# Kernel optimization log

Hardware: AMD Instinct MI355X
Metric: run time of the kernel (lower is better)

The kernel has to match this reference:

```python
import jax, jax.numpy as jnp
import numpy as np

HEADS = 4
KNN_K = 20
BN_EPS = 1e-5


def conv1x1(w, b, x):
    # 1x1 Conv1d: w [out, in], x [B, in, N] -> [B, out, N]
    return jnp.einsum('oc,bcn->bon', w, x) + b[None, :, None]


def setup_inputs() -> dict:
    key = jax.random.key(0)
    B, C, N = 2, 128, 2048
    ks = jax.random.split(key, 16)
    W = lambda k, o, i: jax.random.normal(k, (o, i), jnp.float32) * 0.05
    V = lambda k, o: jax.random.normal(k, (o,), jnp.float32) * 0.05
    return {
        'desc1': jax.random.normal(ks[0], (B, C, N, 1), jnp.float32),
        'wq': W(ks[1], C, C), 'bq': V(ks[2], C),
        'wk': W(ks[3], C, C), 'bk': V(ks[4], C),
        'wv': W(ks[5], C, C), 'bv': V(ks[6], C),
        'wm': W(ks[7], C, C), 'bm': V(ks[8], C),
        'w1': W(ks[9], 2 * C, 2 * C), 'b1': V(ks[10], 2 * C),
        'gamma': jnp.ones((2 * C,), jnp.float32),
        'beta': jnp.zeros((2 * C,), jnp.float32),
        'w2': W(ks[11], C, 2 * C), 'b2': V(ks[12], C),
    }


def reference(desc1, wq, bq, wk, bk, wv, bv, wm, bm, w1, b1, gamma, beta, w2, b2):
    x = desc1[..., 0]                      # [B, C, N]
    B, C, N = x.shape
    D = C // HEADS

    q = conv1x1(wq, bq, x).reshape(B, HEADS, D, N)
    k = conv1x1(wk, bk, x).reshape(B, HEADS, D, N)
    v = conv1x1(wv, bv, x).reshape(B, HEADS, D, N)

    # kNN on raw descriptors: pd = -||xi||^2 + 2 xi.xj - ||xj||^2 (larger = closer)
    xx = jnp.sum(x * x, axis=1)            # [B, N]
    pd = 2.0 * jnp.einsum('bcn,bcm->bnm', x, x) - xx[:, :, None] - xx[:, None, :]
    idx = jax.lax.top_k(pd, KNN_K)[1]      # [B, N, K]

    # scatter ones at kNN indices, then keep only mutual neighbors
    bI = jnp.arange(B)[:, None, None]
    nI = jnp.arange(N)[None, :, None]
    mask = jnp.zeros((B, N, N), x.dtype).at[bI, nI, idx].set(1.0)
    mask = mask * mask.transpose(0, 2, 1)  # [B, N, N]

    score = jnp.einsum('bhdn,bhdm->bhnm', q, k) / (D ** 0.5)
    m = mask[:, None]                      # broadcast over heads
    score = score * m + (-1e9) * (1.0 - m)
    score = jax.nn.softmax(score, axis=-1)

    av = jnp.einsum('bhnm,bhdm->bhdn', score, v).reshape(B, C, N)
    av = conv1x1(wm, bm, av)

    h = conv1x1(w1, b1, jnp.concatenate([x, av], axis=1))  # [B, 2C, N]
    mu = jnp.mean(h, axis=(0, 2), keepdims=True)
    var = jnp.var(h, axis=(0, 2), keepdims=True)           # biased, matches torch BN
    h = (h - mu) / jnp.sqrt(var + BN_EPS) * gamma[None, :, None] + beta[None, :, None]
    h = jax.nn.relu(h)

    out = x + conv1x1(w2, b2, h)
    return out[..., None]                  # [B, C, N, 1]
```

## Files before the change

### kernel.cpp

```cpp
#include <hip/hip_runtime.h>
#include <math.h>

#define NPT 2048
#define KNN 20

typedef const float* fp;
typedef __attribute__((ext_vector_type(4))) float f32x4;
typedef __attribute__((ext_vector_type(8))) short s16x8;

__device__ __forceinline__ ushort f2bf_rne(float v) {
    unsigned u = __float_as_uint(v);
    unsigned r = u + 0x7FFFu + ((u >> 16) & 1u);
    return (ushort)(r >> 16);
}
__device__ __forceinline__ float bfbits2f(ushort h) {
    return __uint_as_float(((unsigned)h) << 16);
}
__device__ __forceinline__ s16x8 ldfrag(const ushort* p) {
    union { uint4 u; s16x8 s; } cv;
    cv.u = *reinterpret_cast<const uint4*>(p);
    return cv.s;
}
__device__ __forceinline__ void f8_hilo(const float* row, s16x8* hi, s16x8* lo) {
    float4 f0 = *reinterpret_cast<const float4*>(row);
    float4 f1 = *reinterpret_cast<const float4*>(row + 4);
    float f[8] = {f0.x, f0.y, f0.z, f0.w, f1.x, f1.y, f1.z, f1.w};
    union { ushort u[8]; s16x8 s; } H, L;
    #pragma unroll
    for (int j = 0; j < 8; j++) {
        ushort h = f2bf_rne(f[j]);
        H.u[j] = h;
        L.u[j] = f2bf_rne(f[j] - bfbits2f(h));
    }
    *hi = H.s; *lo = L.s;
}

__global__ __launch_bounds__(256) void prep_all(
    fp xbf, fp wq, fp wk, fp wv, fp wm, fp w1, fp w2, fp bm, fp b1,
    float* xx, ushort* xhiF, ushort* xloF,
    ushort* wqFhi, ushort* wqFlo, ushort* wkFhi, ushort* wkFlo,
    ushort* wvFhi, ushort* wvFlo,
    ushort* wcFhi, ushort* wcFlo, ushort* w2Fhi, ushort* w2Flo,
    float* b1p, float* stats) {
    int t = threadIdx.x;
    if (blockIdx.x < 256) {
        __shared__ float xs[16][129];
        __shared__ float xpart[16][17];
        int p0 = blockIdx.x * 16;
        int b = p0 >> 11, n0 = p0 & 2047;
        fp xb = xbf + (size_t)b * 128 * NPT;
        {
            int c = t >> 1, half = t & 1;
            float4 f0 = *reinterpret_cast<const float4*>(xb + (size_t)c * NPT + n0 + half * 8);
            float4 f1 = *reinterpret_cast<const float4*>(xb + (size_t)c * NPT + n0 + half * 8 + 4);
            xs[half * 8 + 0][c] = f0.x; xs[half * 8 + 1][c] = f0.y;
            xs[half * 8 + 2][c] = f0.z; xs[half * 8 + 3][c] = f0.w;
            xs[half * 8 + 4][c] = f1.x; xs[half * 8 + 5][c] = f1.y;
            xs[half * 8 + 6][c] = f1.z; xs[half * 8 + 7][c] = f1.w;
        }
        __syncthreads();
        int p = t & 15, g = t >> 4, c0 = g * 8;
        float f[8];
        #pragma unroll
        for (int j = 0; j < 8; j++) f[j] = xs[p][c0 + j];
        float ps = 0.f;
        #pragma unroll
        for (int j = 0; j < 8; j++) ps += f[j] * f[j];
        xpart[p][g] = ps;
        union { ushort u[8]; uint4 q; } H, L;
        #pragma unroll
        for (int j = 0; j < 8; j++) {
            ushort hi = f2bf_rne(f[j]);
            H.u[j] = hi;
            L.u[j] = f2bf_rne(f[j] - bfbits2f(hi));
        }
        size_t off = ((size_t)blockIdx.x * 4 + (c0 >> 5)) * 512
                   + (size_t)(((((c0 >> 3) & 3) * 16) + p) * 8);
        *reinterpret_cast<uint4*>(xhiF + off) = H.q;
        *reinterpret_cast<uint4*>(xloF + off) = L.q;
        __syncthreads();
        if (t < 16) {
            float s = 0.f;
            #pragma unroll
            for (int gg = 0; gg < 16; gg++) s += xpart[t][gg];
            xx[p0 + t] = s;
        }
        return;
    }
    int wid = (blockIdx.x - 256) * 256 + t;
    if (wid < 49152) {
        int which = wid >> 14, e = wid & 16383;
        int lane = (e >> 3) & 63, j = e & 7, kk = (e >> 9) & 3, nt = e >> 11;
        int n = nt * 16 + (lane & 15);
        int k = kk * 32 + (lane >> 4) * 8 + j;
        fp src = which == 0 ? wq : which == 1 ? wk : wv;
        float v = src[n * 128 + k];
        ushort hi = f2bf_rne(v);
        (which == 0 ? wqFhi : which == 1 ? wkFhi : wvFhi)[e] = hi;
        (which == 0 ? wqFlo : which == 1 ? wkFlo : wvFlo)[e] = f2bf_rne(v - bfbits2f(hi));
    } else if (wid < 114688) {
        int e = wid - 49152;
        int j = e & 7, lane = (e >> 3) & 63, kk = (e >> 9) & 7, nt = e >> 12;
        int n = nt * 16 + (lane & 15);
        int k = kk * 32 + (lane >> 4) * 8 + j;
        float v;
        if (k < 128) {
            v = w1[n * 256 + k];
        } else {
            int c = k - 128;
            float s = 0.f;
            for (int i = 0; i < 128; i += 4) {
                float4 wr = *reinterpret_cast<const float4*>(w1 + n * 256 + 128 + i);
                s += wr.x * wm[(i + 0) * 128 + c];
                s += wr.y * wm[(i + 1) * 128 + c];
                s += wr.z * wm[(i + 2) * 128 + c];
                s += wr.w * wm[(i + 3) * 128 + c];
            }
            v = s;
        }
        ushort hi = f2bf_rne(v);
        wcFhi[e] = hi;
        wcFlo[e] = f2bf_rne(v - bfbits2f(hi));
    } else if (wid < 147456) {
        int e = wid - 114688;
        int j = e & 7, lane = (e >> 3) & 63, kk = (e >> 9) & 7, nt = e >> 12;
        int n = nt * 16 + (lane & 15);
        int k = kk * 32 + (lane >> 4) * 8 + j;
        float v = w2[n * 256 + k];
        ushort hi = f2bf_rne(v);
        w2Fhi[e] = hi;
        w2Flo[e] = f2bf_rne(v - bfbits2f(hi));
    } else if (wid < 147712) {
        int o = wid - 147456;
        float s = b1[o];
        for (int i = 0; i < 128; i++)
            s += w1[o * 256 + 128 + i] * bm[i];
        b1p[o] = s;
    } else {
        stats[wid - 147712] = 0.0f;
    }
}

#define MERGE(off) { float ov = __shfl_xor(bv, off); int oi = __shfl_xor(bi, off); \
                     if (ov > bv || (ov == bv && oi < bi)) { bv = ov; bi = oi; } }

#define KEYTILE(C, DST) { \
    int ctl = half * 64 + w * 4 + C; \
    int ct = slab * 128 + ctl; \
    f32x4 a = (f32x4){0.f, 0.f, 0.f, 0.f}; \
    _Pragma("unroll 2") \
    for (int kk = 0; kk < 4; kk++) { \
        s16x8 ah = ldfrag(Ahi[kk] + lane * 8); \
        s16x8 al = ldfrag(Alo[kk] + lane * 8); \
        s16x8 bh = ldfrag(xhiF + ((size_t)(ct * 4 + kk)) * 512 + lane * 8); \
        s16x8 bl = ldfrag(xloF + ((size_t)(ct * 4 + kk)) * 512 + lane * 8); \
        a = __builtin_amdgcn_mfma_f32_16x16x32_bf16(ah, bh, a, 0, 0, 0); \
        a = __builtin_amdgcn_mfma_f32_16x16x32_bf16(al, bh, a, 0, 0, 0); \
        a = __builtin_amdgcn_mfma_f32_16x16x32_bf16(ah, bl, a, 0, 0, 0); \
    } \
    float xxc = xx[slab * 2048 + ctl * 16 + cl]; \
    a[0] = 2.0f * a[0] - xxc; a[1] = 2.0f * a[1] - xxc; \
    a[2] = 2.0f * a[2] - xxc; a[3] = 2.0f * a[3] - xxc; \
    DST = a; \
}

__global__ __launch_bounds__(1024, 8) void gemm_key_topk(
    const ushort* xhiF, const ushort* xloF, const float* xx,
    const ushort* wqFhi, const ushort* wqFlo,
    const ushort* wkFhi, const ushort* wkFlo,
    const ushort* wvFhi, const ushort* wvFlo,
    fp bq, fp bk, fp bv_, float* qT, float* kT, float* vT,
    float* pvv, int* pii, int* cntb, float* scratch) {
    __shared__ ushort Ahi[4][512];
    __shared__ ushort Alo[4][512];
    __shared__ float chm[16][32];
    __shared__ float sv[16][256];
    __shared__ int   si[16][256];
    __shared__ float Trow[16];
    __shared__ int   rowcnt[16];
    __shared__ int   ovfAll;
    int tt = threadIdx.x, w = tt >> 6, lane = tt & 63;
    int rt = blockIdx.x >> 1, half = blockIdx.x & 1;
    int slab = rt >> 7, rtl = rt & 127;
    int cl = lane & 15, quad = lane >> 4;

    if (tt < 16) rowcnt[tt] = 0;

    if (tt < 512) {
        int which = tt >> 8, kk = (tt >> 6) & 3, ln = tt & 63;
        const ushort* src = (which ? xloF : xhiF)
                          + ((size_t)(rt * 4 + kk)) * 512 + ln * 8;
        uint4 v = *reinterpret_cast<const uint4*>(src);
        *reinterpret_cast<uint4*>((which ? Alo[kk] : Ahi[kk]) + ln * 8) = v;
    }
    __syncthreads();

    if (w < 12) {
        int pair = half * 12 + w;
        int mat = pair >> 3, nt = pair & 7;
        const ushort* whi = mat == 0 ? wqFhi : mat == 1 ? wkFhi : wvFhi;
        const ushort* wlo = mat == 0 ? wqFlo : mat == 1 ? wkFlo : wvFlo;
        f32x4 acc = (f32x4){0.f, 0.f, 0.f, 0.f};
        #pragma unroll 2
        for (int kk = 0; kk < 4; kk++) {
            s16x8 ah = ldfrag(Ahi[kk] + lane * 8);
            s16x8 al = ldfrag(Alo[kk] + lane * 8);
            s16x8 bhi = ldfrag(whi + ((size_t)(nt * 4 + kk)) * 512 + lane * 8);
            s16x8 blo = ldfrag(wlo + ((size_t)(nt * 4 + kk)) * 512 + lane * 8);
            acc = __builtin_amdgcn_mfma_f32_16x16x32_bf16(ah, bhi, acc, 0, 0, 0);
            acc = __builtin_amdgcn_mfma_f32_16x16x32_bf16(al, bhi, acc, 0, 0, 0);
            acc = __builtin_amdgcn_mfma_f32_16x16x32_bf16(ah, blo, acc, 0, 0, 0);
        }
        int p0 = rt * 16;
        fp bias    = mat == 0 ? bq : mat == 1 ? bk : bv_;
        float* out = mat == 0 ? qT : mat == 1 ? kT : vT;
        int o = nt * 16 + cl;
        float bvv = bias[o];
        #pragma unroll
        for (int r = 0; r < 4; r++)
            out[(size_t)(p0 + quad * 4 + r) * 128 + o] = acc[r] + bvv;
    }
    __builtin_amdgcn_sched_barrier(0);

    f32x4 key0, key1, key2, key3;
    KEYTILE(0, key0)
    __builtin_amdgcn_sched_barrier(0);
    KEYTILE(1, key1)
    __builtin_amdgcn_sched_barrier(0);
    KEYTILE(2, key2)
    __builtin_amdgcn_sched_barrier(0);
    KEYTILE(3, key3)
    __builtin_amdgcn_sched_barrier(0);

    {
        float m[4];
        #pragma unroll
        for (int r = 0; r < 4; r++) {
            float mm = fmaxf(fmaxf(key0[r], key1[r]), fmaxf(key2[r], key3[r]));
            mm = fmaxf(mm, __shfl_xor(mm, 1));
            mm = fmaxf(mm, __shfl_xor(mm, 2));
            mm = fmaxf(mm, __shfl_xor(mm, 4));
            m[r] = mm;
        }
        if ((cl & 7) == 0) {
            #pragma unroll
            for (int r = 0; r < 4; r++)
                chm[quad * 4 + r][w * 2 + (cl >> 3)] = m[r];
        }
    }
    __syncthreads();

    {
        float bs = (lane < 32) ? chm[w][lane] : -3.4e38f;
        #pragma unroll
        for (int k = 2; k <= 64; k <<= 1) {
            #pragma unroll
            for (int j = k >> 1; j > 0; j >>= 1) {
                float o = __shfl_xor(bs, j);
                bool dirDesc = (lane & k) != 0;
                bool upper   = (lane & j) != 0;
                bs = (upper != dirDesc) ? fmaxf(bs, o) : fminf(bs, o);
            }
        }
        float T = __shfl(bs, 44);
        if (lane == 0) Trow[w] = T;
    }
    __syncthreads();

    #pragma unroll
    for (int r = 0; r < 4; r++) {
        int row = quad * 4 + r;
        float T = Trow[row];
        float vals[4] = {key0[r], key1[r], key2[r], key3[r]};
        #pragma unroll
        for (int c = 0; c < 4; c++) {
            float v = vals[c];
            if (v >= T) {
                int pos = atomicAdd(&rowcnt[row], 1);
                if (pos < 256) {
                    sv[row][pos] = v;
                    si[row][pos] = (half * 64 + w * 4 + c) * 16 + cl;
                }
            }
        }
    }
    __syncthreads();
    if (tt == 0) {
        int o = 0;
        for (int i = 0; i < 16; i++) o |= (rowcnt[i] > 256) ? 1 : 0;
        ovfAll = o;
    }
    __syncthreads();
    int ovf = ovfAll;

    int S = rowcnt[w];
    int rowg = slab * 2048 + rtl * 16 + w;
    size_t sbase = ((size_t)rowg * 2 + half) * 256;
    if (S <= 256) {
        if (lane == 0) cntb[rowg * 2 + half] = S;
        for (int g = lane; g < S; g += 64) {
            pvv[sbase + g] = sv[w][g];
            pii[sbase + g] = si[w][g];
        }
    }

    if (ovf) {
        #pragma unroll
        for (int r = 0; r < 4; r++) {
            float vals[4] = {key0[r], key1[r], key2[r], key3[r]};
            #pragma unroll
            for (int c = 0; c < 4; c++)
                scratch[((size_t)rt * 16 + quad * 4 + r) * 2048
                        + (half * 64 + w * 4 + c) * 16 + cl] = vals[c];
        }
        __syncthreads();
        if (rowcnt[w] > 256) {
            const float* rowp = scratch + ((size_t)rt * 16 + w) * 2048 + half * 1024;
            float rv[16];
            #pragma unroll
            for (int j = 0; j < 16; j++) rv[j] = rowp[j * 64 + lane];
            unsigned removed = 0u;
            for (int iter = 0; iter < KNN; iter++) {
                float bv = -3.4e38f; int bi = 0;
                #pragma unroll
                for (int sl = 0; sl < 16; sl++) {
                    bool live = ((removed >> sl) & 1u) == 0u;
                    if (live && rv[sl] > bv) {
                        bv = rv[sl]; bi = half * 1024 + sl * 64 + lane;
                    }
                }
                MERGE(32) MERGE(16) MERGE(8) MERGE(4) MERGE(2) MERGE(1)
                if (lane == 0) { pvv[sbase + iter] = bv; pii[sbase + iter] = bi; }
                if ((bi & 63) == lane) removed |= 1u << ((bi - half * 1024) >> 6);
            }
            if (lane == 0) cntb[rowg * 2 + half] = -1;
        }
    }
}

__global__ __launch_bounds__(256) void sort_topk(
    const float* pvv, const int* pii, const int* cntb, int* idxbuf) {
    int w = threadIdx.x >> 6, lane = threadIdx.x & 63;
    int row = blockIdx.x * 4 + w;
    int c0 = cntb[row * 2 + 0], c1 = cntb[row * 2 + 1];
    if (c0 < 0) c0 = KNN;
    if (c1 < 0) c1 = KNN;
    int Stot = c0 + c1;
    const float* v0 = pvv + ((size_t)row * 2 + 0) * 256;
    const float* v1 = pvv + ((size_t)row * 2 + 1) * 256;
    const int*   i0 = pii + ((size_t)row * 2 + 0) * 256;
    const int*   i1 = pii + ((size_t)row * 2 + 1) * 256;
    if (Stot <= 64) {
        float v; int idx;
        if (lane < c0)        { v = v0[lane];      idx = i0[lane]; }
        else if (lane < Stot) { v = v1[lane - c0]; idx = i1[lane - c0]; }
        else                  { v = -3.4e38f;      idx = 0x7FFFFFFF; }
        #pragma unroll
        for (int k = 2; k <= 64; k <<= 1) {
            #pragma unroll
            for (int j = k >> 1; j > 0; j >>= 1) {
                float ov = __shfl_xor(v, j); int oi = __shfl_xor(idx, j);
                bool dirDesc = (lane & k) != 0;
                bool upper   = (lane & j) != 0;
                bool takeMax = (upper != dirDesc);
                bool amax = (v > ov) || (v == ov && idx < oi);
                if (takeMax != amax) { v = ov; idx = oi; }
            }
        }
        if (lane >= 44) idxbuf[(size_t)row * KNN + (63 - lane)] = idx;
    } else {
        float vl[8]; int il[8];
        #pragma unroll
        for (int s = 0; s < 8; s++) {
            int g = lane + s * 64;
            float v = -3.4e38f; int idx = 0x7FFFFFFF;
            if (g < c0)        { v = v0[g];      idx = i0[g]; }
            else if (g < Stot) { v = v1[g - c0]; idx = i1[g - c0]; }
            vl[s] = v; il[s] = idx;
        }
        unsigned removed = 0u;
        for (int iter = 0; iter < KNN; iter++) {
            float bv = -3.4e38f; int bi = 0x7FFFFFFF;
            #pragma unroll
            for (int s = 0; s < 8; s++) {
                bool live = ((removed >> s) & 1u) == 0u;
                if (live && (vl[s] > bv || (vl[s] == bv && il[s] < bi))) {
                    bv = vl[s]; bi = il[s];
                }
            }
            MERGE(32) MERGE(16) MERGE(8) MERGE(4) MERGE(2) MERGE(1)
            if (lane == 0) idxbuf[(size_t)row * KNN + iter] = bi;
            #pragma unroll
            for (int s = 0; s < 8; s++)
                if (il[s] == bi) removed |= 1u << s;
        }
    }
}

__global__ __launch_bounds__(256) void k3_attn(
    fp qT, fp kT, fp vT, const int* idxbuf, float* avT) {
    __shared__ float sbuf[2][KNN * 4];
    __shared__ int   mlist[2][KNN];
    __shared__ int   cnt_s[2];
    int tt = threadIdx.x;
    int half = tt >> 7, t = tt & 127;
    int p = blockIdx.x * 2 + half;
    int b = p >> 11, n = p & 2047;
    int bbase = b * NPT;
    int h = t >> 5;

    if ((tt >> 6) == half * 2) {
        int lane = tt & 63;
        bool fl = false; int m = 0;
        if (lane < KNN) {
            m = idxbuf[(size_t)p * KNN + lane] & 2047;
            const int4* mrow = reinterpret_cast<const int4*>(idxbuf + (size_t)(bbase + m) * KNN);
            int4 r0 = mrow[0], r1 = mrow[1], r2 = mrow[2], r3 = mrow[3], r4 = mrow[4];
            fl = (r0.x == n) || (r0.y == n) || (r0.z == n) || (r0.w == n)
              || (r1.x == n) || (r1.y == n) || (r1.z == n) || (r1.w == n)
              || (r2.x == n) || (r2.y == n) || (r2.z == n) || (r2.w == n)
              || (r3.x == n) || (r3.y == n) || (r3.z == n) || (r3.w == n)
              || (r4.x == n) || (r4.y == n) || (r4.z == n) || (r4.w == n);
        }
        unsigned long long mask = __ballot(fl);
        int pos = __popcll(mask & ((1ull << lane) - 1ull));
        if (fl) mlist[half][pos] = m;
        if (lane == 0) cnt_s[half] = (int)__popcll(mask);
    }
    __syncthreads();

    int cnt = cnt_s[half];
    float qv = qT[(size_t)p * 128 + t];
    for (int jj = 0; jj < cnt; jj++) {
        int m = mlist[half][jj];
        float prod = qv * kT[(size_t)(bbase + m) * 128 + t];
        prod += __shfl_xor(prod, 16);
        prod += __shfl_xor(prod, 8);
        prod += __shfl_xor(prod, 4);
        prod += __shfl_xor(prod, 2);
        prod += __shfl_xor(prod, 1);
        if ((t & 31) == 0) sbuf[half][jj * 4 + h] = prod * 0.17677669529663687f;
    }
    __syncthreads();

    float mx = -3.4e38f;
    for (int j = 0; j < cnt; j++) mx = fmaxf(mx, sbuf[half][j * 4 + h]);
    float den = 0.f;
    for (int j = 0; j < cnt; j++) den += expf(sbuf[half][j * 4 + h] - mx);
    float inv = (cnt > 0) ? (1.0f / den) : 0.0f;
    float acc = 0.f;
    for (int j = 0; j < cnt; j++) {
        float pw = expf(sbuf[half][j * 4 + h] - mx) * inv;
        acc += pw * vT[(size_t)(bbase + mlist[half][j]) * 128 + t];
    }
    avT[(size_t)p * 128 + t] = acc;
}

__global__ __launch_bounds__(1024) void k4b_h(
    const ushort* xhiF, const ushort* xloF, const float* avT,
    const ushort* wcFhi, const ushort* wcFlo,
    const float* b1p, float* hbuf, float* stats) {
    __shared__ ushort AH[8][512];
    __shared__ ushort AL[8][512];
    int tt = threadIdx.x, w = tt >> 6, lane = tt & 63;
    int rt = blockIdx.x;
    int p0 = rt * 16;

    if (w < 8) {
        int which = w & 1, kk = w >> 1;
        const ushort* src = (which ? xloF : xhiF)
                          + ((size_t)(rt * 4 + kk)) * 512 + lane * 8;
        uint4 v = *reinterpret_cast<const uint4*>(src);
        *reinterpret_cast<uint4*>((which ? AL[kk] : AH[kk]) + lane * 8) = v;
    } else if (w < 12) {
        int kk = 4 + (w - 8);
        const float* arow = avT + (size_t)(p0 + (lane & 15)) * 128
                          + (kk - 4) * 32 + (lane >> 4) * 8;
        s16x8 hi, lo;
        f8_hilo(arow, &hi, &lo);
        union { s16x8 s; uint4 u; } cvh, cvl;
        cvh.s = hi; cvl.s = lo;
        *reinterpret_cast<uint4*>(AH[kk] + lane * 8) = cvh.u;
        *reinterpret_cast<uint4*>(AL[kk] + lane * 8) = cvl.u;
    }
    __syncthreads();

    int nt = w;
    f32x4 acc = (f32x4){0.f, 0.f, 0.f, 0.f};
    for (int kk = 0; kk < 8; kk++) {
        s16x8 ahi = ldfrag(AH[kk] + lane * 8);
        s16x8 alo = ldfrag(AL[kk] + lane * 8);
        s16x8 bhi = ldfrag(wcFhi + ((size_t)(nt * 8 + kk)) * 512 + lane * 8);
        s16x8 blo = ldfrag(wcFlo + ((size_t)(nt * 8 + kk)) * 512 + lane * 8);
        acc = __builtin_amdgcn_mfma_f32_16x16x32_bf16(ahi, bhi, acc, 0, 0, 0);
        acc = __builtin_amdgcn_mfma_f32_16x16x32_bf16(alo, bhi, acc, 0, 0, 0);
        acc = __builtin_amdgcn_mfma_f32_16x16x32_bf16(ahi, blo, acc, 0, 0, 0);
    }

    int cl = lane & 15, quad = lane >> 4;
    int o = nt * 16 + cl;
    float bb = b1p[o];
    float s = 0.f, s2 = 0.f;
    #pragma unroll
    for (int r = 0; r < 4; r++) {
        float v = acc[r] + bb;
        hbuf[(size_t)(p0 + quad * 4 + r) * 256 + o] = v;
        s += v; s2 += v * v;
    }
    s  += __shfl_xor(s, 16);  s  += __shfl_xor(s, 32);
    s2 += __shfl_xor(s2, 16); s2 += __shfl_xor(s2, 32);
    if (quad == 0) {
        atomicAdd(&stats[o], s);
        atomicAdd(&stats[256 + o], s2);
    }
}

__global__ __launch_bounds__(512) void k5b_out(
    const float* hbuf, const float* stats, fp gamma, fp beta,
    const ushort* w2Fhi, const ushort* w2Flo,
    fp b2, fp xbf, float* out) {
    __shared__ ushort HH[8][512];
    __shared__ ushort HL[8][512];
    int tt = threadIdx.x, w = tt >> 6, lane = tt & 63;
    int rt = blockIdx.x;
    int p0 = rt * 16;

    {
        int kk = w;
        int c0 = kk * 32 + (lane >> 4) * 8;
        const float* hrow = hbuf + (size_t)(p0 + (lane & 15)) * 256 + c0;
        float4 f0 = *reinterpret_cast<const float4*>(hrow);
        float4 f1 = *reinterpret_cast<const float4*>(hrow + 4);
        float4 s0 = *reinterpret_cast<const float4*>(stats + c0);
        float4 s1 = *reinterpret_cast<const float4*>(stats + c0 + 4);
        float4 q0 = *reinterpret_cast<const float4*>(stats + 256 + c0);
        float4 q1 = *reinterpret_cast<const float4*>(stats + 256 + c0 + 4);
        float4 g0 = *reinterpret_cast<const float4*>(gamma + c0);
        float4 g1 = *reinterpret_cast<const float4*>(gamma + c0 + 4);
        float4 e0 = *reinterpret_cast<const float4*>(beta + c0);
        float4 e1 = *reinterpret_cast<const float4*>(beta + c0 + 4);
        float f[8] = {f0.x, f0.y, f0.z, f0.w, f1.x, f1.y, f1.z, f1.w};
        float sm[8] = {s0.x, s0.y, s0.z, s0.w, s1.x, s1.y, s1.z, s1.w};
        float sq[8] = {q0.x, q0.y, q0.z, q0.w, q1.x, q1.y, q1.z, q1.w};
        float gm[8] = {g0.x, g0.y, g0.z, g0.w, g1.x, g1.y, g1.z, g1.w};
        float bt[8] = {e0.x, e0.y, e0.z, e0.w, e1.x, e1.y, e1.z, e1.w};
        union { ushort u[8]; uint4 q; } H, L;
        #pragma unroll
        for (int j = 0; j < 8; j++) {
            float mu  = sm[j] * (1.0f / 4096.0f);
            float var = fmaxf(sq[j] * (1.0f / 4096.0f) - mu * mu, 0.0f);
            float a    = gm[j] / sqrtf(var + 1e-5f);
            float cadd = bt[j] - mu * a;
            float v = fmaxf(f[j] * a + cadd, 0.0f);
            ushort hi = f2bf_rne(v);
            H.u[j] = hi;
            L.u[j] = f2bf_rne(v - bfbits2f(hi));
        }
        *reinterpret_cast<uint4*>(HH[kk] + lane * 8) = H.q;
        *reinterpret_cast<uint4*>(HL[kk] + lane * 8) = L.q;
    }
    __syncthreads();

    int nt = w;
    f32x4 acc = (f32x4){0.f, 0.f, 0.f, 0.f};
    for (int kk = 0; kk < 8; kk++) {
        s16x8 ahi = ldfrag(HH[kk] + lane * 8);
        s16x8 alo = ldfrag(HL[kk] + lane * 8);
        s16x8 bhi = ldfrag(w2Fhi + ((size_t)(nt * 8 + kk)) * 512 + lane * 8);
        s16x8 blo = ldfrag(w2Flo + ((size_t)(nt * 8 + kk)) * 512 + lane * 8);
        acc = __builtin_amdgcn_mfma_f32_16x16x32_bf16(ahi, bhi, acc, 0, 0, 0);
        acc = __builtin_amdgcn_mfma_f32_16x16x32_bf16(alo, bhi, acc, 0, 0, 0);
        acc = __builtin_amdgcn_mfma_f32_16x16x32_bf16(ahi, blo, acc, 0, 0, 0);
    }
    int cl = lane & 15, quad = lane >> 4;
    int b = p0 >> 11, n0 = p0 & 2047;
    int o = nt * 16 + cl;
    float bb = b2[o];
    size_t base = (size_t)b * 128 * NPT + (size_t)o * NPT + n0 + quad * 4;
    float4 xv = *reinterpret_cast<const float4*>(xbf + base);
    float4 ov;
    ov.x = acc[0] + bb + xv.x;
    ov.y = acc[1] + bb + xv.y;
    ov.z = acc[2] + bb + xv.z;
    ov.w = acc[3] + bb + xv.w;
    *reinterpret_cast<float4*>(out + base) = ov;
}

#define WS_FULL 61788160u

extern "C" void kernel_launch(void* const* d_in, const int* in_sizes, int n_in,
                              void* d_out, int out_size, void* d_ws, size_t ws_size,
                              hipStream_t stream) {
    fp desc1 = (fp)d_in[0];
    fp wq = (fp)d_in[1];  fp bq = (fp)d_in[2];
    fp wk = (fp)d_in[3];  fp bk = (fp)d_in[4];
    fp wv = (fp)d_in[5];  fp bv = (fp)d_in[6];
    fp wm = (fp)d_in[7];  fp bm = (fp)d_in[8];
    fp w1 = (fp)d_in[9];  fp b1 = (fp)d_in[10];
    fp gamma = (fp)d_in[11]; fp beta = (fp)d_in[12];
    fp w2 = (fp)d_in[13]; fp b2 = (fp)d_in[14];

    if (ws_size < (size_t)WS_FULL) return;

    char* ws = (char*)d_ws;
    float*  qT    = (float*) (ws + 0);
    float*  kT    = (float*) (ws + 2097152);
    float*  vT    = (float*) (ws + 4194304);
    float*  avT   = (float*) (ws + 6291456);
    float*  xx    = (float*) (ws + 8388608);
    int*    idxb  = (int*)   (ws + 8404992);
    float*  stats = (float*) (ws + 8732672);
    float*  b1p   = (float*) (ws + 8734720);
    ushort* wqFhi = (ushort*)(ws + 8736768);
    ushort* wqFlo = (ushort*)(ws + 8769536);
    ushort* wkFhi = (ushort*)(ws + 8802304);
    ushort* wkFlo = (ushort*)(ws + 8835072);
    ushort* wvFhi = (ushort*)(ws + 8867840);
    ushort* wvFlo = (ushort*)(ws + 8900608);
    ushort* wcFhi = (ushort*)(ws + 8933376);
    ushort* wcFlo = (ushort*)(ws + 9064448);
    ushort* w2Fhi = (ushort*)(ws + 9195520);
    ushort* w2Flo = (ushort*)(ws + 9261056);
    ushort* xhiF  = (ushort*)(ws + 9326592);
    ushort* xloF  = (ushort*)(ws + 10375168);
    int*    cntb  = (int*)   (ws + 11423744);
    float*  pvv   = (float*) (ws + 11456512);
    int*    pii   = (int*)   (ws + 19845120);
    float*  scratch = (float*)(ws + 28233728);
    float*  hbuf  = (float*) (ws + 0);

    prep_all<<<835, 256, 0, stream>>>(desc1, wq, wk, wv, wm, w1, w2, bm, b1,
                                      xx, xhiF, xloF,
                                      wqFhi, wqFlo, wkFhi, wkFlo, wvFhi, wvFlo,
                                      wcFhi, wcFlo, w2Fhi, w2Flo, b1p, stats);
    gemm_key_topk<<<512, 1024, 0, stream>>>(xhiF, xloF, xx,
                                            wqFhi, wqFlo, wkFhi, wkFlo,
                                            wvFhi, wvFlo,
                                            bq, bk, bv, qT, kT, vT,
                                            pvv, pii, cntb, scratch);
    sort_topk<<<1024, 256, 0, stream>>>(pvv, pii, cntb, idxb);
    k3_attn<<<2048, 256, 0, stream>>>(qT, kT, vT, idxb, avT);
    k4b_h<<<256, 1024, 0, stream>>>(xhiF, xloF, avT, wcFhi, wcFlo,
                                    b1p, hbuf, stats);
    k5b_out<<<256, 512, 0, stream>>>(hbuf, stats, gamma, beta, w2Fhi, w2Flo,
                                     b2, desc1, (float*)d_out);
}
```

Measured before the change: 186.1 us.

## Merge half-row key blocks into one block covering full 2048-column row

Each gemm_key_topk block now computes all 2048 key columns for its 16 rows instead of splitting them across two blocks. Each wave handles two column tiles per MFMA pass, sharing the A fragments. The threshold now comes from 64 chunk maxima instead of 32, and each row writes a single candidate list, so sort_topk no longer merges two halves. The grid halves to 256 blocks with launch bounds lowered to 4, which trades parallelism and occupancy for fewer redundant A loads and a cheaper merge stage, plus possibly more candidates per row.

```diff
diff --git a/kernel.cpp b/kernel.cpp
--- a/kernel.cpp
+++ b/kernel.cpp
@@ -144,27 +144,36 @@
 #define MERGE(off) { float ov = __shfl_xor(bv, off); int oi = __shfl_xor(bi, off); \
                      if (ov > bv || (ov == bv && oi < bi)) { bv = ov; bi = oi; } }
 
-#define KEYTILE(C, DST) { \
-    int ctl = half * 64 + w * 4 + C; \
-    int ct = slab * 128 + ctl; \
-    f32x4 a = (f32x4){0.f, 0.f, 0.f, 0.f}; \
+#define KEYPAIR(C0, D0, D1) { \
+    int ct0 = slab * 128 + w * 8 + C0; \
+    int ct1 = ct0 + 1; \
+    f32x4 a0 = (f32x4){0.f, 0.f, 0.f, 0.f}; \
+    f32x4 a1 = (f32x4){0.f, 0.f, 0.f, 0.f}; \
     _Pragma("unroll 2") \
     for (int kk = 0; kk < 4; kk++) { \
         s16x8 ah = ldfrag(Ahi[kk] + lane * 8); \
         s16x8 al = ldfrag(Alo[kk] + lane * 8); \
-        s16x8 bh = ldfrag(xhiF + ((size_t)(ct * 4 + kk)) * 512 + lane * 8); \
-        s16x8 bl = ldfrag(xloF + ((size_t)(ct * 4 + kk)) * 512 + lane * 8); \
-        a = __builtin_amdgcn_mfma_f32_16x16x32_bf16(ah, bh, a, 0, 0, 0); \
-        a = __builtin_amdgcn_mfma_f32_16x16x32_bf16(al, bh, a, 0, 0, 0); \
-        a = __builtin_amdgcn_mfma_f32_16x16x32_bf16(ah, bl, a, 0, 0, 0); \
+        s16x8 b0h = ldfrag(xhiF + ((size_t)(ct0 * 4 + kk)) * 512 + lane * 8); \
+        s16x8 b0l = ldfrag(xloF + ((size_t)(ct0 * 4 + kk)) * 512 + lane * 8); \
+        s16x8 b1h = ldfrag(xhiF + ((size_t)(ct1 * 4 + kk)) * 512 + lane * 8); \
+        s16x8 b1l = ldfrag(xloF + ((size_t)(ct1 * 4 + kk)) * 512 + lane * 8); \
+        a0 = __builtin_amdgcn_mfma_f32_16x16x32_bf16(ah, b0h, a0, 0, 0, 0); \
+        a1 = __builtin_amdgcn_mfma_f32_16x16x32_bf16(ah, b1h, a1, 0, 0, 0); \
+        a0 = __builtin_amdgcn_mfma_f32_16x16x32_bf16(al, b0h, a0, 0, 0, 0); \
+        a1 = __builtin_amdgcn_mfma_f32_16x16x32_bf16(al, b1h, a1, 0, 0, 0); \
+        a0 = __builtin_amdgcn_mfma_f32_16x16x32_bf16(ah, b0l, a0, 0, 0, 0); \
+        a1 = __builtin_amdgcn_mfma_f32_16x16x32_bf16(ah, b1l, a1, 0, 0, 0); \
     } \
-    float xxc = xx[slab * 2048 + ctl * 16 + cl]; \
-    a[0] = 2.0f * a[0] - xxc; a[1] = 2.0f * a[1] - xxc; \
-    a[2] = 2.0f * a[2] - xxc; a[3] = 2.0f * a[3] - xxc; \
-    DST = a; \
-}
-
-__global__ __launch_bounds__(1024, 8) void gemm_key_topk(
+    float xx0 = xx[slab * 2048 + (w * 8 + C0) * 16 + cl]; \
+    float xx1 = xx[slab * 2048 + (w * 8 + C0 + 1) * 16 + cl]; \
+    a0[0] = 2.0f * a0[0] - xx0; a0[1] = 2.0f * a0[1] - xx0; \
+    a0[2] = 2.0f * a0[2] - xx0; a0[3] = 2.0f * a0[3] - xx0; \
+    a1[0] = 2.0f * a1[0] - xx1; a1[1] = 2.0f * a1[1] - xx1; \
+    a1[2] = 2.0f * a1[2] - xx1; a1[3] = 2.0f * a1[3] - xx1; \
+    D0 = a0; D1 = a1; \
+}
+
+__global__ __launch_bounds__(1024, 4) void gemm_key_topk(
     const ushort* xhiF, const ushort* xloF, const float* xx,
     const ushort* wqFhi, const ushort* wqFlo,
     const ushort* wkFhi, const ushort* wkFlo,
@@ -173,14 +182,14 @@
     float* pvv, int* pii, int* cntb, float* scratch) {
     __shared__ ushort Ahi[4][512];
     __shared__ ushort Alo[4][512];
-    __shared__ float chm[16][32];
+    __shared__ float chm[16][64];
     __shared__ float sv[16][256];
     __shared__ int   si[16][256];
     __shared__ float Trow[16];
     __shared__ int   rowcnt[16];
     __shared__ int   ovfAll;
     int tt = threadIdx.x, w = tt >> 6, lane = tt & 63;
-    int rt = blockIdx.x >> 1, half = blockIdx.x & 1;
+    int rt = blockIdx.x;
     int slab = rt >> 7, rtl = rt & 127;
     int cl = lane & 15, quad = lane >> 4;
 
@@ -196,62 +205,82 @@
     __syncthreads();
 
     if (w < 12) {
-        int pair = half * 12 + w;
-        int mat = pair >> 3, nt = pair & 7;
-        const ushort* whi = mat == 0 ? wqFhi : mat == 1 ? wkFhi : wvFhi;
-        const ushort* wlo = mat == 0 ? wqFlo : mat == 1 ? wkFlo : wvFlo;
-        f32x4 acc = (f32x4){0.f, 0.f, 0.f, 0.f};
+        f32x4 acc0 = (f32x4){0.f, 0.f, 0.f, 0.f};
+        f32x4 acc1 = (f32x4){0.f, 0.f, 0.f, 0.f};
+        int pair0 = w * 2, pair1 = w * 2 + 1;
+        int mat0 = pair0 >> 3, nt0 = pair0 & 7;
+        int mat1 = pair1 >> 3, nt1 = pair1 & 7;
+        const ushort* w0hi = mat0 == 0 ? wqFhi : mat0 == 1 ? wkFhi : wvFhi;
+        const ushort* w0lo = mat0 == 0 ? wqFlo : mat0 == 1 ? wkFlo : wvFlo;
+        const ushort* w1hi = mat1 == 0 ? wqFhi : mat1 == 1 ? wkFhi : wvFhi;
+        const ushort* w1lo = mat1 == 0 ? wqFlo : mat1 == 1 ? wkFlo : wvFlo;
         #pragma unroll 2
         for (int kk = 0; kk < 4; kk++) {
             s16x8 ah = ldfrag(Ahi[kk] + lane * 8);
             s16x8 al = ldfrag(Alo[kk] + lane * 8);
-            s16x8 bhi = ldfrag(whi + ((size_t)(nt * 4 + kk)) * 512 + lane * 8);
-            s16x8 blo = ldfrag(wlo + ((size_t)(nt * 4 + kk)) * 512 + lane * 8);
-            acc = __builtin_amdgcn_mfma_f32_16x16x32_bf16(ah, bhi, acc, 0, 0, 0);
-            acc = __builtin_amdgcn_mfma_f32_16x16x32_bf16(al, bhi, acc, 0, 0, 0);
-            acc = __builtin_amdgcn_mfma_f32_16x16x32_bf16(ah, blo, acc, 0, 0, 0);
+            s16x8 b0h = ldfrag(w0hi + ((size_t)(nt0 * 4 + kk)) * 512 + lane * 8);
+            s16x8 b0l = ldfrag(w0lo + ((size_t)(nt0 * 4 + kk)) * 512 + lane * 8);
+            s16x8 b1h = ldfrag(w1hi + ((size_t)(nt1 * 4 + kk)) * 512 + lane * 8);
+            s16x8 b1l = ldfrag(w1lo + ((size_t)(nt1 * 4 + kk)) * 512 + lane * 8);
+            acc0 = __builtin_amdgcn_mfma_f32_16x16x32_bf16(ah, b0h, acc0, 0, 0, 0);
+            acc1 = __builtin_amdgcn_mfma_f32_16x16x32_bf16(ah, b1h, acc1, 0, 0, 0);
+            acc0 = __builtin_amdgcn_mfma_f32_16x16x32_bf16(al, b0h, acc0, 0, 0, 0);
+            acc1 = __builtin_amdgcn_mfma_f32_16x16x32_bf16(al, b1h, acc1, 0, 0, 0);
+            acc0 = __builtin_amdgcn_mfma_f32_16x16x32_bf16(ah, b0l, acc0, 0, 0, 0);
+            acc1 = __builtin_amdgcn_mfma_f32_16x16x32_bf16(ah, b1l, acc1, 0, 0, 0);
         }
         int p0 = rt * 16;
-        fp bias    = mat == 0 ? bq : mat == 1 ? bk : bv_;
-        float* out = mat == 0 ? qT : mat == 1 ? kT : vT;
-        int o = nt * 16 + cl;
-        float bvv = bias[o];
-        #pragma unroll
-        for (int r = 0; r < 4; r++)
-            out[(size_t)(p0 + quad * 4 + r) * 128 + o] = acc[r] + bvv;
+        {
+            fp bias    = mat0 == 0 ? bq : mat0 == 1 ? bk : bv_;
+            float* out = mat0 == 0 ? qT : mat0 == 1 ? kT : vT;
+            int o = nt0 * 16 + cl;
+            float bvv = bias[o];
+            #pragma unroll
+            for (int r = 0; r < 4; r++)
+                out[(size_t)(p0 + quad * 4 + r) * 128 + o] = acc0[r] + bvv;
+        }
+        {
+            fp bias    = mat1 == 0 ? bq : mat1 == 1 ? bk : bv_;
+            float* out = mat1 == 0 ? qT : mat1 == 1 ? kT : vT;
+            int o = nt1 * 16 + cl;
+            float bvv = bias[o];
+            #pragma unroll
+            for (int r = 0; r < 4; r++)
+                out[(size_t)(p0 + quad * 4 + r) * 128 + o] = acc1[r] + bvv;
+        }
     }
     __builtin_amdgcn_sched_barrier(0);
 
-    f32x4 key0, key1, key2, key3;
-    KEYTILE(0, key0)
+    f32x4 key0, key1, key2, key3, key4, key5, key6, key7;
+    KEYPAIR(0, key0, key1)
     __builtin_amdgcn_sched_barrier(0);
-    KEYTILE(1, key1)
+    KEYPAIR(2, key2, key3)
     __builtin_amdgcn_sched_barrier(0);
-    KEYTILE(2, key2)
+    KEYPAIR(4, key4, key5)
     __builtin_amdgcn_sched_barrier(0);
-    KEYTILE(3, key3)
+    KEYPAIR(6, key6, key7)
     __builtin_amdgcn_sched_barrier(0);
 
     {
         float m[4];
         #pragma unroll
         for (int r = 0; r < 4; r++) {
-            float mm = fmaxf(fmaxf(key0[r], key1[r]), fmaxf(key2[r], key3[r]));
+            float mm = fmaxf(fmaxf(fmaxf(key0[r], key1[r]), fmaxf(key2[r], key3[r])),
+                             fmaxf(fmaxf(key4[r], key5[r]), fmaxf(key6[r], key7[r])));
             mm = fmaxf(mm, __shfl_xor(mm, 1));
             mm = fmaxf(mm, __shfl_xor(mm, 2));
-            mm = fmaxf(mm, __shfl_xor(mm, 4));
             m[r] = mm;
         }
-        if ((cl & 7) == 0) {
+        if ((cl & 3) == 0) {
             #pragma unroll
             for (int r = 0; r < 4; r++)
-                chm[quad * 4 + r][w * 2 + (cl >> 3)] = m[r];
+                chm[quad * 4 + r][w * 4 + (cl >> 2)] = m[r];
         }
     }
     __syncthreads();
 
     {
-        float bs = (lane < 32) ? chm[w][lane] : -3.4e38f;
+        float bs = chm[w][lane];
         #pragma unroll
         for (int k = 2; k <= 64; k <<= 1) {
             #pragma unroll
@@ -271,15 +300,16 @@
     for (int r = 0; r < 4; r++) {
         int row = quad * 4 + r;
         float T = Trow[row];
-        float vals[4] = {key0[r], key1[r], key2[r], key3[r]};
-        #pragma unroll
-        for (int c = 0; c < 4; c++) {
+        float vals[8] = {key0[r], key1[r], key2[r], key3[r],
+                         key4[r], key5[r], key6[r], key7[r]};
+        #pragma unroll
+        for (int c = 0; c < 8; c++) {
             float v = vals[c];
             if (v >= T) {
                 int pos = atomicAdd(&rowcnt[row], 1);
                 if (pos < 256) {
                     sv[row][pos] = v;
-                    si[row][pos] = (half * 64 + w * 4 + c) * 16 + cl;
+                    si[row][pos] = (w * 8 + c) * 16 + cl;
                 }
             }
         }
@@ -295,9 +325,9 @@
 
     int S = rowcnt[w];
     int rowg = slab * 2048 + rtl * 16 + w;
-    size_t sbase = ((size_t)rowg * 2 + half) * 256;
+    size_t sbase = (size_t)rowg * 256;
     if (S <= 256) {
-        if (lane == 0) cntb[rowg * 2 + half] = S;
+        if (lane == 0) cntb[rowg] = S;
         for (int g = lane; g < S; g += 64) {
             pvv[sbase + g] = sv[w][g];
             pii[sbase + g] = si[w][g];
@@ -307,33 +337,32 @@
     if (ovf) {
         #pragma unroll
         for (int r = 0; r < 4; r++) {
-            float vals[4] = {key0[r], key1[r], key2[r], key3[r]};
-            #pragma unroll
-            for (int c = 0; c < 4; c++)
+            float vals[8] = {key0[r], key1[r], key2[r], key3[r],
+                             key4[r], key5[r], key6[r], key7[r]};
+            #pragma unroll
+            for (int c = 0; c < 8; c++)
                 scratch[((size_t)rt * 16 + quad * 4 + r) * 2048
-                        + (half * 64 + w * 4 + c) * 16 + cl] = vals[c];
+                        + (w * 8 + c) * 16 + cl] = vals[c];
         }
         __syncthreads();
         if (rowcnt[w] > 256) {
-            const float* rowp = scratch + ((size_t)rt * 16 + w) * 2048 + half * 1024;
-            float rv[16];
-            #pragma unroll
-            for (int j = 0; j < 16; j++) rv[j] = rowp[j * 64 + lane];
+            const float* rowp = scratch + ((size_t)rt * 16 + w) * 2048;
+            float rv[32];
+            #pragma unroll
+            for (int j = 0; j < 32; j++) rv[j] = rowp[j * 64 + lane];
             unsigned removed = 0u;
             for (int iter = 0; iter < KNN; iter++) {
                 float bv = -3.4e38f; int bi = 0;
                 #pragma unroll
-                for (int sl = 0; sl < 16; sl++) {
+                for (int sl = 0; sl < 32; sl++) {
                     bool live = ((removed >> sl) & 1u) == 0u;
-                    if (live && rv[sl] > bv) {
-                        bv = rv[sl]; bi = half * 1024 + sl * 64 + lane;
-                    }
+                    if (live && rv[sl] > bv) { bv = rv[sl]; bi = sl * 64 + lane; }
                 }
                 MERGE(32) MERGE(16) MERGE(8) MERGE(4) MERGE(2) MERGE(1)
                 if (lane == 0) { pvv[sbase + iter] = bv; pii[sbase + iter] = bi; }
-                if ((bi & 63) == lane) removed |= 1u << ((bi - half * 1024) >> 6);
+                if ((bi & 63) == lane) removed |= 1u << (bi >> 6);
             }
-            if (lane == 0) cntb[rowg * 2 + half] = -1;
+            if (lane == 0) cntb[rowg] = -1;
         }
     }
 }
@@ -342,19 +371,14 @@
     const float* pvv, const int* pii, const int* cntb, int* idxbuf) {
     int w = threadIdx.x >> 6, lane = threadIdx.x & 63;
     int row = blockIdx.x * 4 + w;
-    int c0 = cntb[row * 2 + 0], c1 = cntb[row * 2 + 1];
-    if (c0 < 0) c0 = KNN;
-    if (c1 < 0) c1 = KNN;
-    int Stot = c0 + c1;
-    const float* v0 = pvv + ((size_t)row * 2 + 0) * 256;
-    const float* v1 = pvv + ((size_t)row * 2 + 1) * 256;
-    const int*   i0 = pii + ((size_t)row * 2 + 0) * 256;
-    const int*   i1 = pii + ((size_t)row * 2 + 1) * 256;
-    if (Stot <= 64) {
+    int S = cntb[row];
+    if (S < 0) S = KNN;
+    const float* v0 = pvv + (size_t)row * 256;
+    const int*   i0 = pii + (size_t)row * 256;
+    if (S <= 64) {
         float v; int idx;
-        if (lane < c0)        { v = v0[lane];      idx = i0[lane]; }
-        else if (lane < Stot) { v = v1[lane - c0]; idx = i1[lane - c0]; }
-        else                  { v = -3.4e38f;      idx = 0x7FFFFFFF; }
+        if (lane < S) { v = v0[lane]; idx = i0[lane]; }
+        else          { v = -3.4e38f; idx = 0x7FFFFFFF; }
         #pragma unroll
         for (int k = 2; k <= 64; k <<= 1) {
             #pragma unroll
@@ -369,20 +393,19 @@
         }
         if (lane >= 44) idxbuf[(size_t)row * KNN + (63 - lane)] = idx;
     } else {
-        float vl[8]; int il[8];
-        #pragma unroll
-        for (int s = 0; s < 8; s++) {
+        float vl[4]; int il[4];
+        #pragma unroll
+        for (int s = 0; s < 4; s++) {
             int g = lane + s * 64;
-            float v = -3.4e38f; int idx = 0x7FFFFFFF;
-            if (g < c0)        { v = v0[g];      idx = i0[g]; }
-            else if (g < Stot) { v = v1[g - c0]; idx = i1[g - c0]; }
-            vl[s] = v; il[s] = idx;
+            bool ok = g < S;
+            vl[s] = ok ? v0[g] : -3.4e38f;
+            il[s] = ok ? i0[g] : 0x7FFFFFFF;
         }
         unsigned removed = 0u;
         for (int iter = 0; iter < KNN; iter++) {
             float bv = -3.4e38f; int bi = 0x7FFFFFFF;
             #pragma unroll
-            for (int s = 0; s < 8; s++) {
+            for (int s = 0; s < 4; s++) {
                 bool live = ((removed >> s) & 1u) == 0u;
                 if (live && (vl[s] > bv || (vl[s] == bv && il[s] < bi))) {
                     bv = vl[s]; bi = il[s];
@@ -391,7 +414,7 @@
             MERGE(32) MERGE(16) MERGE(8) MERGE(4) MERGE(2) MERGE(1)
             if (lane == 0) idxbuf[(size_t)row * KNN + iter] = bi;
             #pragma unroll
-            for (int s = 0; s < 8; s++)
+            for (int s = 0; s < 4; s++)
                 if (il[s] == bi) removed |= 1u << s;
         }
     }
@@ -586,7 +609,7 @@
     *reinterpret_cast<float4*>(out + base) = ov;
 }
 
-#define WS_FULL 61788160u
+#define WS_FULL 53383168u
 
 extern "C" void kernel_launch(void* const* d_in, const int* in_sizes, int n_in,
                               void* d_out, int out_size, void* d_ws, size_t ws_size,
@@ -624,16 +647,16 @@
     ushort* xhiF  = (ushort*)(ws + 9326592);
     ushort* xloF  = (ushort*)(ws + 10375168);
     int*    cntb  = (int*)   (ws + 11423744);
-    float*  pvv   = (float*) (ws + 11456512);
-    int*    pii   = (int*)   (ws + 19845120);
-    float*  scratch = (float*)(ws + 28233728);
+    float*  pvv   = (float*) (ws + 11440128);
+    int*    pii   = (int*)   (ws + 15634432);
+    float*  scratch = (float*)(ws + 19828736);
     float*  hbuf  = (float*) (ws + 0);
 
     prep_all<<<835, 256, 0, stream>>>(desc1, wq, wk, wv, wm, w1, w2, bm, b1,
                                       xx, xhiF, xloF,
                                       wqFhi, wqFlo, wkFhi, wkFlo, wvFhi, wvFlo,
                                       wcFhi, wcFlo, w2Fhi, w2Flo, b1p, stats);
-    gemm_key_topk<<<512, 1024, 0, stream>>>(xhiF, xloF, xx,
+    gemm_key_topk<<<256, 1024, 0, stream>>>(xhiF, xloF, xx,
                                             wqFhi, wqFlo, wkFhi, wkFlo,
                                             wvFhi, wvFlo,
                                             bq, bk, bv, qT, kT, vT,
```

Measured after the change: 156.7 us. -15.8%, faster.
